# Optimization experiments

Measured on AMD Instinct MI355X. Metric: run time of the kernel, lower is better.

The kernel has to match this reference:

```python
import jax, jax.numpy as jnp
import numpy as np

N, E, DIM, H = 50000, 800000, 128, 8
HD = DIM // H  # head_dim = 16
HID = 4 * DIM  # ffn hidden (hidden_dim_multiplier=4)


def setup_inputs() -> dict:
    key = jax.random.key(0)
    ks = jax.random.split(key, 12)
    s = 0.05
    return {
        "x": jax.random.normal(ks[0], (N, DIM), jnp.float32),
        "src": jax.random.randint(ks[1], (E,), 0, N, jnp.int32),
        "dst": jax.random.randint(ks[2], (E,), 0, N, jnp.int32),
        "fc_w": jax.random.normal(ks[3], (DIM, DIM), jnp.float32) * s,
        "fc_b": jax.random.normal(ks[4], (DIM,), jnp.float32) * s,
        "au_w": jax.random.normal(ks[5], (H, DIM), jnp.float32) * s,
        "au_b": jax.random.normal(ks[6], (H,), jnp.float32) * s,
        "av_w": jax.random.normal(ks[7], (H, DIM), jnp.float32) * s,
        "w1": jax.random.normal(ks[8], (HID, 4 * DIM), jnp.float32) * s,
        "b1": jax.random.normal(ks[9], (HID,), jnp.float32) * s,
        "w2": jax.random.normal(ks[10], (DIM, HID), jnp.float32) * s,
        "b2": jax.random.normal(ks[11], (DIM,), jnp.float32) * s,
    }


def reference(x, src, dst, fc_w, fc_b, au_w, au_b, av_w, w1, b1, w2, b2):
    h = x @ fc_w.T + fc_b                                   # [N, DIM]
    su = h @ au_w.T + au_b                                  # [N, H]
    sv = h @ av_w.T                                         # [N, H] (no bias)
    # u_add_v + LeakyReLU(0.2)
    scores = jax.nn.leaky_relu(su[src] + sv[dst], 0.2)      # [E, H]
    # edge_softmax grouped by destination node (stable)
    m = jax.ops.segment_max(scores, dst, num_segments=N)    # [N, H]
    ex = jnp.exp(scores - m[dst])
    den = jax.ops.segment_sum(ex, dst, num_segments=N)      # [N, H]
    probs = ex / den[dst]                                   # [E, H]
    # u_mul_e_sum over heads: x reshaped [N, head_dim, H]
    xh = h.reshape(N, HD, H)
    msg = jax.ops.segment_sum(xh[src] * probs[:, None, :], dst, num_segments=N)
    msg = msg.reshape(N, DIM)
    # copy_u_mean: mean of src features over incoming edges
    ones = jnp.ones((E,), h.dtype)
    in_deg = jax.ops.segment_sum(ones, dst, num_segments=N)   # [N]
    sum2 = jax.ops.segment_sum(xh[src], dst, num_segments=N)  # [N, HD, H]
    msg2 = (sum2 / jnp.maximum(in_deg, 1.0)[:, None, None]).reshape(N, DIM)
    # symmetric-norm message: norm = 1/sqrt(out_deg[src]*out_deg[dst])
    out_deg = jax.ops.segment_sum(ones, src, num_segments=N)  # [N]
    norm = 1.0 / jnp.sqrt(out_deg[src] * out_deg[dst])        # [E]
    msg3 = jax.ops.segment_sum(h[src] * norm[:, None], dst, num_segments=N)
    # combine + feed-forward (dropout=0 -> identity)
    cat = jnp.concatenate([h, msg, msg2, msg3], axis=1)       # [N, 4*DIM]
    f = jax.nn.gelu(cat @ w1.T + b1, approximate=False)
    return f @ w2.T + b2                                      # [N, DIM]
```

## Files before the change

### kernel.cpp

```cpp
#include <hip/hip_runtime.h>
#include <hip/hip_bf16.h>

#define NNODES 50000
#define NEDGES 800000
#define DIM 128
#define NH 8
#define HID 512
#define NB 196

typedef unsigned short ushort_t;
typedef unsigned int uint_t;
typedef __attribute__((ext_vector_type(8))) short bf16x8;
typedef __attribute__((ext_vector_type(4))) float f32x4;

__global__ __launch_bounds__(256) void convert_weights_kernel(
    const float* __restrict__ fc_w, const float* __restrict__ w1,
    const float* __restrict__ w2,
    ushort_t* __restrict__ fc_wb, ushort_t* __restrict__ w1b,
    ushort_t* __restrict__ w2b)
{
    int i = blockIdx.x * 256 + threadIdx.x;
    if (i < 16384)
        ((__hip_bfloat16*)fc_wb)[i] = __float2bfloat16(fc_w[i]);
    else if (i < 278528)
        ((__hip_bfloat16*)w1b)[i - 16384] = __float2bfloat16(w1[i - 16384]);
    else if (i < 344064)
        ((__hip_bfloat16*)w2b)[i - 278528] = __float2bfloat16(w2[i - 278528]);
}

template<int AF32, int OUTF32, int ACT>
__global__ __launch_bounds__(256, 3) void gemm_mfma(
    const void* A, int lda,
    const ushort_t* __restrict__ B, int ldb,
    const float* __restrict__ bias,
    void* C, int ldc, int row0,
    int M, int K)
{
    constexpr int BM = 128, BN = 128, BK = 32, PAD = 8;
    __shared__ ushort_t As[BM][BK + PAD];
    __shared__ ushort_t Bs[BN][BK + PAD];

    const int t    = threadIdx.x;
    const int bm   = blockIdx.y * BM;
    const int bn   = blockIdx.x * BN;
    const int wid  = t >> 6, lane = t & 63;
    const int wrow = wid >> 1, wcol = wid & 1;
    const int qd   = lane >> 4, l16 = lane & 15;

    f32x4 acc[4][4];
#pragma unroll
    for (int i = 0; i < 4; ++i)
#pragma unroll
        for (int j = 0; j < 4; ++j) acc[i][j] = (f32x4){0.f, 0.f, 0.f, 0.f};

    for (int k0 = 0; k0 < K; k0 += BK) {
#pragma unroll
        for (int i = 0; i < 2; ++i) {
            int v = t + i * 256;
            int r = v >> 2, c8 = (v & 3) * 8;
            int gr = bm + r;
            if (AF32) {
                float4 f0 = make_float4(0.f, 0.f, 0.f, 0.f), f1 = f0;
                if (gr < M) {
                    const float* ap = (const float*)A + (size_t)gr * lda + k0 + c8;
                    f0 = *(const float4*)ap;
                    f1 = *(const float4*)(ap + 4);
                }
                __hip_bfloat16* dstp = (__hip_bfloat16*)&As[r][c8];
                dstp[0] = __float2bfloat16(f0.x); dstp[1] = __float2bfloat16(f0.y);
                dstp[2] = __float2bfloat16(f0.z); dstp[3] = __float2bfloat16(f0.w);
                dstp[4] = __float2bfloat16(f1.x); dstp[5] = __float2bfloat16(f1.y);
                dstp[6] = __float2bfloat16(f1.z); dstp[7] = __float2bfloat16(f1.w);
            } else {
                uint4 val = make_uint4(0u, 0u, 0u, 0u);
                if (gr < M) val = *(const uint4*)((const ushort_t*)A + (size_t)gr * lda + k0 + c8);
                *(uint4*)(&As[r][c8]) = val;
            }
        }
#pragma unroll
        for (int i = 0; i < 2; ++i) {
            int v = t + i * 256;
            int r = v >> 2, c8 = (v & 3) * 8;
            *(uint4*)(&Bs[r][c8]) = *(const uint4*)(B + (size_t)(bn + r) * ldb + k0 + c8);
        }
        __syncthreads();

        bf16x8 af[4], bfr[4];
#pragma unroll
        for (int mi = 0; mi < 4; ++mi)
            af[mi] = *(const bf16x8*)(&As[wrow * 64 + mi * 16 + l16][qd * 8]);
#pragma unroll
        for (int ni = 0; ni < 4; ++ni)
            bfr[ni] = *(const bf16x8*)(&Bs[wcol * 64 + ni * 16 + l16][qd * 8]);
#pragma unroll
        for (int mi = 0; mi < 4; ++mi)
#pragma unroll
            for (int ni = 0; ni < 4; ++ni)
                acc[mi][ni] = __builtin_amdgcn_mfma_f32_16x16x32_bf16(
                    af[mi], bfr[ni], acc[mi][ni], 0, 0, 0);
        __syncthreads();
    }

#pragma unroll
    for (int mi = 0; mi < 4; ++mi) {
#pragma unroll
        for (int r = 0; r < 4; ++r) {
            int lrow = wrow * 64 + mi * 16 + qd * 4 + r;
            int grow = bm + lrow;
            if (grow >= M) continue;
#pragma unroll
            for (int ni = 0; ni < 4; ++ni) {
                int gc = bn + wcol * 64 + ni * 16 + l16;
                float v = acc[mi][ni][r] + bias[gc];
                if (ACT == 1) v = 0.5f * v * (1.f + erff(v * 0.70710678118654752f));
                size_t off = (size_t)(row0 + grow) * ldc + gc;
                if (OUTF32) ((float*)C)[off] = v;
                else ((__hip_bfloat16*)C)[off] = __float2bfloat16(v);
            }
        }
    }
}

__global__ __launch_bounds__(256) void attn_scores_kernel(
    const ushort_t* __restrict__ hb,
    const float* __restrict__ au_w, const float* __restrict__ au_b,
    const float* __restrict__ av_w,
    float* __restrict__ su, float* __restrict__ sv, int N)
{
    const int wave = threadIdx.x >> 6;
    const int lane = threadIdx.x & 63;
    const int n = blockIdx.x * 4 + wave;
    if (n >= N) return;

    const float h0 = __bfloat162float(((const __hip_bfloat16*)hb)[(size_t)n * DIM + lane]);
    const float h1 = __bfloat162float(((const __hip_bfloat16*)hb)[(size_t)n * DIM + 64 + lane]);

    float au[NH], av[NH];
#pragma unroll
    for (int hh = 0; hh < NH; ++hh) {
        au[hh] = h0 * au_w[hh * DIM + lane] + h1 * au_w[hh * DIM + 64 + lane];
        av[hh] = h0 * av_w[hh * DIM + lane] + h1 * av_w[hh * DIM + 64 + lane];
    }
#pragma unroll
    for (int off = 32; off >= 1; off >>= 1) {
#pragma unroll
        for (int hh = 0; hh < NH; ++hh) {
            au[hh] += __shfl_down(au[hh], off, 64);
            av[hh] += __shfl_down(av[hh], off, 64);
        }
    }
    if (lane == 0) {
#pragma unroll
        for (int hh = 0; hh < NH; ++hh) {
            su[(size_t)n * NH + hh] = au[hh] + au_b[hh];
            sv[(size_t)n * NH + hh] = av[hh];
        }
    }
}

__global__ __launch_bounds__(256) void degree_count_kernel(
    const int* __restrict__ src, const int* __restrict__ dst,
    float* __restrict__ out_deg, int* __restrict__ in_cnt, int E)
{
    int e = blockIdx.x * 256 + threadIdx.x;
    if (e >= E) return;
    unsafeAtomicAdd(&out_deg[src[e]], 1.f);
    atomicAdd(&in_cnt[dst[e]], 1);
}

__global__ __launch_bounds__(256) void block_sum_kernel(
    const int* __restrict__ cnt, int* __restrict__ bsum)
{
    const int lane = threadIdx.x & 63, wid = threadIdx.x >> 6;
    int i = blockIdx.x * 256 + threadIdx.x;
    int v = (i < NNODES) ? cnt[i] : 0;
#pragma unroll
    for (int off = 32; off >= 1; off >>= 1) v += __shfl_down(v, off, 64);
    __shared__ int ws_[4];
    if (lane == 0) ws_[wid] = v;
    __syncthreads();
    if (threadIdx.x == 0) bsum[blockIdx.x] = ws_[0] + ws_[1] + ws_[2] + ws_[3];
}

__global__ __launch_bounds__(256) void block_scan_kernel(
    const int* __restrict__ bsum, int* __restrict__ boff)
{
    __shared__ int sb[256];
    const int t = threadIdx.x;
    int v = (t < NB) ? bsum[t] : 0;
    sb[t] = v;
    __syncthreads();
    for (int off = 1; off < 256; off <<= 1) {
        int u = (t >= off) ? sb[t - off] : 0;
        __syncthreads();
        sb[t] += u;
        __syncthreads();
    }
    if (t < NB) boff[t] = (t == 0) ? 0 : sb[t - 1];
}

__global__ __launch_bounds__(256) void final_scan_kernel(
    const int* __restrict__ cnt, const int* __restrict__ boff,
    int* __restrict__ rowstart)
{
    __shared__ int sb[256];
    const int t = threadIdx.x;
    const int b = blockIdx.x;
    int i = b * 256 + t;
    int v = (i < NNODES) ? cnt[i] : 0;
    sb[t] = v;
    __syncthreads();
    for (int off = 1; off < 256; off <<= 1) {
        int u = (t >= off) ? sb[t - off] : 0;
        __syncthreads();
        sb[t] += u;
        __syncthreads();
    }
    if (i < NNODES) rowstart[i] = boff[b] + sb[t] - v;
    if (b == 0 && t == 0) rowstart[NNODES] = NEDGES;
}

__global__ __launch_bounds__(256) void fill_csr_kernel(
    const int* __restrict__ src, const int* __restrict__ dst,
    const int* __restrict__ rowstart, int* __restrict__ cursor,
    int* __restrict__ esrc, int E)
{
    int e = blockIdx.x * 256 + threadIdx.x;
    if (e >= E) return;
    int d = dst[e];
    int pos = rowstart[d] + atomicAdd(&cursor[d], 1);
    esrc[pos] = src[e];
}

__device__ __forceinline__ float bf_lo(uint_t v) {
    union { uint_t i; float f; } c; c.i = v << 16; return c.f;
}
__device__ __forceinline__ float bf_hi(uint_t v) {
    union { uint_t i; float f; } c; c.i = v & 0xffff0000u; return c.f;
}
__device__ __forceinline__ void st_bf2(ushort_t* p, float a, float b) {
    __hip_bfloat16 ba = __float2bfloat16(a), bb = __float2bfloat16(b);
    uint_t v = (uint_t)(*(ushort_t*)&ba) | ((uint_t)(*(ushort_t*)&bb) << 16);
    *(uint_t*)p = v;
}

__global__ __launch_bounds__(256) void gather_aggregate_kernel(
    const int* __restrict__ rowstart, const int* __restrict__ esrc,
    const ushort_t* __restrict__ hb,
    const float* __restrict__ su, const float* __restrict__ sv,
    const float* __restrict__ out_deg,
    ushort_t* __restrict__ cat, int N)
{
    const int wave = threadIdx.x >> 6;
    const int lane = threadIdx.x & 63;
    const int n = blockIdx.x * 4 + wave;
    if (n >= N) return;

    const int d0 = lane << 1;
    const int h0 = d0 & 7;

    const int e0  = rowstart[n];
    const int deg = rowstart[n + 1] - e0;
    const float2 svv = *(const float2*)(sv + (size_t)n * NH + h0);
    const float od_d = out_deg[n];

    int es = 0;
    if (deg > 0) es = esrc[e0 + (lane < deg ? lane : deg - 1)];

    float den0 = 0.f, den1 = 0.f;
    float m0 = 0.f, m1 = 0.f, s0 = 0.f, s1 = 0.f, n0 = 0.f, n1 = 0.f;

    const int degm = deg & ~3;
    for (int j = 0; j < degm; j += 4) {
        int s4[4]; float2 su4[4]; float od4[4]; uint_t hv4[4];
#pragma unroll
        for (int u = 0; u < 4; ++u) {
            int jj = j + u;
            s4[u] = (jj < 64) ? __shfl(es, jj, 64) : esrc[e0 + jj];
        }
#pragma unroll
        for (int u = 0; u < 4; ++u) {
            su4[u] = *(const float2*)(su + (size_t)s4[u] * NH + h0);
            od4[u] = out_deg[s4[u]];
            hv4[u] = *(const uint_t*)(hb + (size_t)s4[u] * DIM + d0);
        }
#pragma unroll
        for (int u = 0; u < 4; ++u) {
            float sc0 = su4[u].x + svv.x; sc0 = sc0 < 0.f ? 0.2f * sc0 : sc0;
            float sc1 = su4[u].y + svv.y; sc1 = sc1 < 0.f ? 0.2f * sc1 : sc1;
            float ex0 = __expf(sc0), ex1 = __expf(sc1);
            den0 += ex0; den1 += ex1;
            float nrm = rsqrtf(od4[u] * od_d);
            float hs0 = bf_lo(hv4[u]), hs1 = bf_hi(hv4[u]);
            m0 += hs0 * ex0; m1 += hs1 * ex1;
            s0 += hs0;       s1 += hs1;
            n0 += hs0 * nrm; n1 += hs1 * nrm;
        }
    }
    for (int j = degm; j < deg; ++j) {
        int s = (j < 64) ? __shfl(es, j, 64) : esrc[e0 + j];
        float2 suv = *(const float2*)(su + (size_t)s * NH + h0);
        float odv  = out_deg[s];
        uint_t hv  = *(const uint_t*)(hb + (size_t)s * DIM + d0);
        float sc0 = suv.x + svv.x; sc0 = sc0 < 0.f ? 0.2f * sc0 : sc0;
        float sc1 = suv.y + svv.y; sc1 = sc1 < 0.f ? 0.2f * sc1 : sc1;
        float ex0 = __expf(sc0), ex1 = __expf(sc1);
        den0 += ex0; den1 += ex1;
        float nrm = rsqrtf(odv * od_d);
        float hs0 = bf_lo(hv), hs1 = bf_hi(hv);
        m0 += hs0 * ex0; m1 += hs1 * ex1;
        s0 += hs0;       s1 += hs1;
        n0 += hs0 * nrm; n1 += hs1 * nrm;
    }

    const float inv = 1.f / fmaxf((float)deg, 1.f);
    const float r0 = den0 > 0.f ? 1.f / den0 : 0.f;
    const float r1 = den1 > 0.f ? 1.f / den1 : 0.f;
    ushort_t* row = cat + (size_t)n * 512;
    *(uint_t*)(row + d0) = *(const uint_t*)(hb + (size_t)n * DIM + d0);
    st_bf2(row + 128 + d0, m0 * r0, m1 * r1);
    st_bf2(row + 256 + d0, s0 * inv, s1 * inv);
    st_bf2(row + 384 + d0, n0, n1);
}

extern "C" void kernel_launch(void* const* d_in, const int* in_sizes, int n_in,
                              void* d_out, int out_size, void* d_ws, size_t ws_size,
                              hipStream_t stream)
{
    const float* x    = (const float*)d_in[0];
    const int*   src  = (const int*)d_in[1];
    const int*   dst  = (const int*)d_in[2];
    const float* fc_w = (const float*)d_in[3];
    const float* fc_b = (const float*)d_in[4];
    const float* au_w = (const float*)d_in[5];
    const float* au_b = (const float*)d_in[6];
    const float* av_w = (const float*)d_in[7];
    const float* w1   = (const float*)d_in[8];
    const float* b1   = (const float*)d_in[9];
    const float* w2   = (const float*)d_in[10];
    const float* b2   = (const float*)d_in[11];
    float* out = (float*)d_out;

    const int N = NNODES, E = NEDGES;

    char* w = (char*)d_ws;
    ushort_t* fc_wb = (ushort_t*)w;  w += (size_t)DIM * DIM * 2;
    ushort_t* w1b   = (ushort_t*)w;  w += (size_t)HID * 512 * 2;
    ushort_t* w2b   = (ushort_t*)w;  w += (size_t)DIM * HID * 2;
    ushort_t* hb    = (ushort_t*)w;  w += (size_t)N * DIM * 2;
    ushort_t* cat   = (ushort_t*)w;  w += (size_t)N * 512 * 2;
    float* su       = (float*)w;     w += (size_t)N * NH * 4;
    float* sv       = (float*)w;     w += (size_t)N * NH * 4;
    float* out_deg  = (float*)w;     w += (size_t)N * 4;
    int*   in_cnt   = (int*)w;       w += (size_t)N * 4;
    int*   cursor   = (int*)w;       w += (size_t)N * 4;
    int*   rowstart = (int*)w;       w += (size_t)(N + 16) * 4;
    int*   bsum     = (int*)w;       w += (size_t)256 * 4;
    int*   boff     = (int*)w;       w += (size_t)256 * 4;
    int*   esrc     = (int*)w;       w += (size_t)E * 4;
    size_t base_bytes = (size_t)(w - (char*)d_ws);
    ushort_t* fbuf  = (ushort_t*)w;

    const int CHR = (ws_size >= base_bytes + (size_t)N * 512 * 2 + 1024) ? N : 12500;

    (void)hipMemsetAsync(out_deg, 0, (size_t)N * 3 * 4, stream);

    convert_weights_kernel<<<1344, 256, 0, stream>>>(fc_w, w1, w2, fc_wb, w1b, w2b);

    {
        dim3 g(1, (N + 127) / 128);
        gemm_mfma<1, 0, 0><<<g, 256, 0, stream>>>(x, DIM, fc_wb, DIM, fc_b,
                                                  hb, DIM, 0, N, DIM);
    }
    attn_scores_kernel<<<(N + 3) / 4, 256, 0, stream>>>(hb, au_w, au_b, av_w, su, sv, N);
    degree_count_kernel<<<(E + 255) / 256, 256, 0, stream>>>(src, dst, out_deg, in_cnt, E);
    block_sum_kernel<<<NB, 256, 0, stream>>>(in_cnt, bsum);
    block_scan_kernel<<<1, 256, 0, stream>>>(bsum, boff);
    final_scan_kernel<<<NB, 256, 0, stream>>>(in_cnt, boff, rowstart);
    fill_csr_kernel<<<(E + 255) / 256, 256, 0, stream>>>(src, dst, rowstart, cursor, esrc, E);
    gather_aggregate_kernel<<<(N + 3) / 4, 256, 0, stream>>>(
        rowstart, esrc, hb, su, sv, out_deg, cat, N);

    for (int c0 = 0; c0 < N; c0 += CHR) {
        int Mc = (c0 + CHR <= N) ? CHR : N - c0;
        {
            dim3 g(HID / 128, (Mc + 127) / 128);
            gemm_mfma<0, 0, 1><<<g, 256, 0, stream>>>(cat + (size_t)c0 * 512, 512,
                                                      w1b, 512, b1,
                                                      fbuf, HID, 0, Mc, 512);
        }
        {
            dim3 g(DIM / 128, (Mc + 127) / 128);
            gemm_mfma<0, 1, 0><<<g, 256, 0, stream>>>(fbuf, HID, w2b, HID, b2,
                                                      out, DIM, c0, Mc, 512);
        }
    }
}
```

Baseline: 439.5 us.

## Double-buffer LDS tiles with register prefetch in the MFMA GEMM

The bf16 MFMA GEMM now keeps two LDS buffers for the A and B tiles. It loads the next K tile into registers while the current tile is being multiplied, then writes it to the other buffer. This removes one of the two block barriers per K step and overlaps global loads with the MFMA work. In exchange, LDS use per block doubles and more registers stay live, which could reduce occupancy.

```diff
diff --git a/kernel.cpp b/kernel.cpp
--- a/kernel.cpp
+++ b/kernel.cpp
@@ -37,8 +37,8 @@
     int M, int K)
 {
     constexpr int BM = 128, BN = 128, BK = 32, PAD = 8;
-    __shared__ ushort_t As[BM][BK + PAD];
-    __shared__ ushort_t Bs[BN][BK + PAD];
+    __shared__ ushort_t As[2][BM][BK + PAD];
+    __shared__ ushort_t Bs[2][BN][BK + PAD];
 
     const int t    = threadIdx.x;
     const int bm   = blockIdx.y * BM;
@@ -53,52 +53,79 @@
 #pragma unroll
         for (int j = 0; j < 4; ++j) acc[i][j] = (f32x4){0.f, 0.f, 0.f, 0.f};
 
-    for (int k0 = 0; k0 < K; k0 += BK) {
+    uint4  pa[2];
+    float4 qa[2][2];
+    uint4  pb[2];
+
+    auto load_regs = [&](int k0) {
 #pragma unroll
         for (int i = 0; i < 2; ++i) {
-            int v = t + i * 256;
-            int r = v >> 2, c8 = (v & 3) * 8;
-            int gr = bm + r;
+            const int v = t + i * 256;
+            const int r = v >> 2, c8 = (v & 3) * 8;
+            const int gr = bm + r;
             if (AF32) {
-                float4 f0 = make_float4(0.f, 0.f, 0.f, 0.f), f1 = f0;
                 if (gr < M) {
                     const float* ap = (const float*)A + (size_t)gr * lda + k0 + c8;
-                    f0 = *(const float4*)ap;
-                    f1 = *(const float4*)(ap + 4);
+                    qa[i][0] = *(const float4*)ap;
+                    qa[i][1] = *(const float4*)(ap + 4);
+                } else {
+                    qa[i][0] = make_float4(0.f, 0.f, 0.f, 0.f);
+                    qa[i][1] = qa[i][0];
                 }
-                __hip_bfloat16* dstp = (__hip_bfloat16*)&As[r][c8];
-                dstp[0] = __float2bfloat16(f0.x); dstp[1] = __float2bfloat16(f0.y);
-                dstp[2] = __float2bfloat16(f0.z); dstp[3] = __float2bfloat16(f0.w);
-                dstp[4] = __float2bfloat16(f1.x); dstp[5] = __float2bfloat16(f1.y);
-                dstp[6] = __float2bfloat16(f1.z); dstp[7] = __float2bfloat16(f1.w);
             } else {
-                uint4 val = make_uint4(0u, 0u, 0u, 0u);
-                if (gr < M) val = *(const uint4*)((const ushort_t*)A + (size_t)gr * lda + k0 + c8);
-                *(uint4*)(&As[r][c8]) = val;
+                pa[i] = (gr < M)
+                    ? *(const uint4*)((const ushort_t*)A + (size_t)gr * lda + k0 + c8)
+                    : make_uint4(0u, 0u, 0u, 0u);
             }
-        }
+            pb[i] = *(const uint4*)(B + (size_t)(bn + r) * ldb + k0 + c8);
+        }
+    };
+
+    auto store_lds = [&](int buf) {
 #pragma unroll
         for (int i = 0; i < 2; ++i) {
-            int v = t + i * 256;
-            int r = v >> 2, c8 = (v & 3) * 8;
-            *(uint4*)(&Bs[r][c8]) = *(const uint4*)(B + (size_t)(bn + r) * ldb + k0 + c8);
-        }
-        __syncthreads();
+            const int v = t + i * 256;
+            const int r = v >> 2, c8 = (v & 3) * 8;
+            if (AF32) {
+                __hip_bfloat16 tmp[8];
+                tmp[0] = __float2bfloat16(qa[i][0].x); tmp[1] = __float2bfloat16(qa[i][0].y);
+                tmp[2] = __float2bfloat16(qa[i][0].z); tmp[3] = __float2bfloat16(qa[i][0].w);
+                tmp[4] = __float2bfloat16(qa[i][1].x); tmp[5] = __float2bfloat16(qa[i][1].y);
+                tmp[6] = __float2bfloat16(qa[i][1].z); tmp[7] = __float2bfloat16(qa[i][1].w);
+                *(uint4*)(&As[buf][r][c8]) = *(const uint4*)tmp;
+            } else {
+                *(uint4*)(&As[buf][r][c8]) = pa[i];
+            }
+            *(uint4*)(&Bs[buf][r][c8]) = pb[i];
+        }
+    };
+
+    const int nk = K / BK;
+    load_regs(0);
+    store_lds(0);
+
+    for (int kb = 0; kb < nk; ++kb) {
+        const int cur = kb & 1;
+        if (kb + 1 < nk) load_regs((kb + 1) * BK);
+
+        asm volatile("s_waitcnt lgkmcnt(0)" ::: "memory");
+        __builtin_amdgcn_s_barrier();
 
         bf16x8 af[4], bfr[4];
 #pragma unroll
         for (int mi = 0; mi < 4; ++mi)
-            af[mi] = *(const bf16x8*)(&As[wrow * 64 + mi * 16 + l16][qd * 8]);
+            af[mi] = *(const bf16x8*)(&As[cur][wrow * 64 + mi * 16 + l16][qd * 8]);
 #pragma unroll
         for (int ni = 0; ni < 4; ++ni)
-            bfr[ni] = *(const bf16x8*)(&Bs[wcol * 64 + ni * 16 + l16][qd * 8]);
+            bfr[ni] = *(const bf16x8*)(&Bs[cur][wcol * 64 + ni * 16 + l16][qd * 8]);
 #pragma unroll
         for (int mi = 0; mi < 4; ++mi)
 #pragma unroll
             for (int ni = 0; ni < 4; ++ni)
                 acc[mi][ni] = __builtin_amdgcn_mfma_f32_16x16x32_bf16(
                     af[mi], bfr[ni], acc[mi][ni], 0, 0, 0);
-        __syncthreads();
+
+        if (kb + 1 < nk) store_lds(cur ^ 1);
     }
 
 #pragma unroll
```

Measured after the change: 481.2 us. 9.5% more time.

## Fuse FFN GEMM1+GELU+GEMM2 into one kernel keeping hidden tile in LDS

Applied to the files above, without the earlier changes.

Replaces the two separate FFN GEMM launches and the global hidden buffer with a single kernel. Each 128-row block computes the hidden activations 128 columns at a time, applies bias and GELU, stores the bf16 tile in shared memory, and immediately accumulates it into the output GEMM. This removes the global write and re-read of the N×512 hidden activations. In exchange each block re-reads the cat row tile four times with no double buffering, reads w2 straight from global memory, and the grid shrinks to about 391 blocks, which lowers parallelism.

```diff
diff --git a/kernel.cpp b/kernel.cpp
--- a/kernel.cpp
+++ b/kernel.cpp
@@ -12,6 +12,11 @@
 typedef unsigned int uint_t;
 typedef __attribute__((ext_vector_type(8))) short bf16x8;
 typedef __attribute__((ext_vector_type(4))) float f32x4;
+
+__device__ __forceinline__ ushort_t f2bf_bits(float v) {
+    __hip_bfloat16 b = __float2bfloat16(v);
+    return *(ushort_t*)&b;
+}
 
 __global__ __launch_bounds__(256) void convert_weights_kernel(
     const float* __restrict__ fc_w, const float* __restrict__ w1,
@@ -121,6 +126,121 @@
     }
 }
 
+__global__ __launch_bounds__(256, 2) void ffn_fused_kernel(
+    const ushort_t* __restrict__ cat,
+    const ushort_t* __restrict__ w1b,
+    const float* __restrict__ b1,
+    const ushort_t* __restrict__ w2b,
+    const float* __restrict__ b2,
+    float* __restrict__ out, int M)
+{
+    constexpr int BM = 128, BK = 32, PAD = 8;
+    __shared__ ushort_t As[BM][BK + PAD];
+    __shared__ ushort_t Bs[128][BK + PAD];
+    __shared__ ushort_t Fs[128][128 + PAD];
+
+    const int t    = threadIdx.x;
+    const int bm   = blockIdx.x * BM;
+    const int wid  = t >> 6, lane = t & 63;
+    const int wrow = wid >> 1, wcol = wid & 1;
+    const int qd   = lane >> 4, l16 = lane & 15;
+
+    f32x4 acc_o[4][4];
+#pragma unroll
+    for (int i = 0; i < 4; ++i)
+#pragma unroll
+        for (int j = 0; j < 4; ++j) acc_o[i][j] = (f32x4){0.f, 0.f, 0.f, 0.f};
+
+    for (int p = 0; p < 4; ++p) {
+        f32x4 acc_f[4][4];
+#pragma unroll
+        for (int i = 0; i < 4; ++i)
+#pragma unroll
+            for (int j = 0; j < 4; ++j) acc_f[i][j] = (f32x4){0.f, 0.f, 0.f, 0.f};
+
+        for (int k0 = 0; k0 < HID; k0 += BK) {
+#pragma unroll
+            for (int i = 0; i < 2; ++i) {
+                int v = t + i * 256;
+                int r = v >> 2, c8 = (v & 3) * 8;
+                int gr = bm + r;
+                uint4 val = make_uint4(0u, 0u, 0u, 0u);
+                if (gr < M) val = *(const uint4*)(cat + (size_t)gr * HID + k0 + c8);
+                *(uint4*)(&As[r][c8]) = val;
+                *(uint4*)(&Bs[r][c8]) =
+                    *(const uint4*)(w1b + (size_t)(p * 128 + r) * HID + k0 + c8);
+            }
+            __syncthreads();
+
+            bf16x8 af[4], bfr[4];
+#pragma unroll
+            for (int mi = 0; mi < 4; ++mi)
+                af[mi] = *(const bf16x8*)(&As[wrow * 64 + mi * 16 + l16][qd * 8]);
+#pragma unroll
+            for (int ni = 0; ni < 4; ++ni)
+                bfr[ni] = *(const bf16x8*)(&Bs[wcol * 64 + ni * 16 + l16][qd * 8]);
+#pragma unroll
+            for (int mi = 0; mi < 4; ++mi)
+#pragma unroll
+                for (int ni = 0; ni < 4; ++ni)
+                    acc_f[mi][ni] = __builtin_amdgcn_mfma_f32_16x16x32_bf16(
+                        af[mi], bfr[ni], acc_f[mi][ni], 0, 0, 0);
+            __syncthreads();
+        }
+
+#pragma unroll
+        for (int mi = 0; mi < 4; ++mi) {
+#pragma unroll
+            for (int r = 0; r < 4; ++r) {
+                int lrow = wrow * 64 + mi * 16 + qd * 4 + r;
+#pragma unroll
+                for (int ni = 0; ni < 4; ++ni) {
+                    int lcol = wcol * 64 + ni * 16 + l16;
+                    float v = acc_f[mi][ni][r] + b1[p * 128 + lcol];
+                    v = 0.5f * v * (1.f + erff(v * 0.70710678118654752f));
+                    Fs[lrow][lcol] = f2bf_bits(v);
+                }
+            }
+        }
+        __syncthreads();
+
+#pragma unroll
+        for (int kk = 0; kk < 4; ++kk) {
+            bf16x8 af2[4], bf2[4];
+#pragma unroll
+            for (int mi = 0; mi < 4; ++mi)
+                af2[mi] = *(const bf16x8*)(&Fs[wrow * 64 + mi * 16 + l16][kk * 32 + qd * 8]);
+#pragma unroll
+            for (int ni = 0; ni < 4; ++ni) {
+                int col2 = wcol * 64 + ni * 16 + l16;
+                bf2[ni] = *(const bf16x8*)(w2b + (size_t)col2 * HID + p * 128 + kk * 32 + qd * 8);
+            }
+#pragma unroll
+            for (int mi = 0; mi < 4; ++mi)
+#pragma unroll
+                for (int ni = 0; ni < 4; ++ni)
+                    acc_o[mi][ni] = __builtin_amdgcn_mfma_f32_16x16x32_bf16(
+                        af2[mi], bf2[ni], acc_o[mi][ni], 0, 0, 0);
+        }
+        __syncthreads();
+    }
+
+#pragma unroll
+    for (int mi = 0; mi < 4; ++mi) {
+#pragma unroll
+        for (int r = 0; r < 4; ++r) {
+            int lrow = wrow * 64 + mi * 16 + qd * 4 + r;
+            int grow = bm + lrow;
+            if (grow >= M) continue;
+#pragma unroll
+            for (int ni = 0; ni < 4; ++ni) {
+                int gc = wcol * 64 + ni * 16 + l16;
+                out[(size_t)grow * DIM + gc] = acc_o[mi][ni][r] + b2[gc];
+            }
+        }
+    }
+}
+
 __global__ __launch_bounds__(256) void attn_scores_kernel(
     const ushort_t* __restrict__ hb,
     const float* __restrict__ au_w, const float* __restrict__ au_b,
@@ -358,10 +478,6 @@
     int*   bsum     = (int*)w;       w += (size_t)256 * 4;
     int*   boff     = (int*)w;       w += (size_t)256 * 4;
     int*   esrc     = (int*)w;       w += (size_t)E * 4;
-    size_t base_bytes = (size_t)(w - (char*)d_ws);
-    ushort_t* fbuf  = (ushort_t*)w;
-
-    const int CHR = (ws_size >= base_bytes + (size_t)N * 512 * 2 + 1024) ? N : 12500;
 
     (void)hipMemsetAsync(out_deg, 0, (size_t)N * 3 * 4, stream);
 
@@ -381,18 +497,6 @@
     gather_aggregate_kernel<<<(N + 3) / 4, 256, 0, stream>>>(
         rowstart, esrc, hb, su, sv, out_deg, cat, N);
 
-    for (int c0 = 0; c0 < N; c0 += CHR) {
-        int Mc = (c0 + CHR <= N) ? CHR : N - c0;
-        {
-            dim3 g(HID / 128, (Mc + 127) / 128);
-            gemm_mfma<0, 0, 1><<<g, 256, 0, stream>>>(cat + (size_t)c0 * 512, 512,
-                                                      w1b, 512, b1,
-                                                      fbuf, HID, 0, Mc, 512);
-        }
-        {
-            dim3 g(DIM / 128, (Mc + 127) / 128);
-            gemm_mfma<0, 1, 0><<<g, 256, 0, stream>>>(fbuf, HID, w2b, HID, b2,
-                                                      out, DIM, c0, Mc, 512);
-        }
-    }
-}
+    ffn_fused_kernel<<<(N + 127) / 128, 256, 0, stream>>>(
+        cat, w1b, b1, w2b, b2, out, N);
+}
```

New measurement: 437.7 us. About the same (-0.4%).
